# Kernel optimization log

Measured on AMD Instinct MI355X. Metric: run time of the kernel, lower is better.

The kernel has to match this reference:

```python
import jax, jax.numpy as jnp
import numpy as np

N = 100000   # nodes
E = 3200000  # edges
D = 16       # n_qubits / feature dim
H = 64       # classifier hidden
C = 10       # output_dims
L = 2        # len(q_depths)


def setup_inputs() -> dict:
    key = jax.random.key(0)
    ks = jax.random.split(key, 16)
    s = 1.0 / np.sqrt(D)
    return {
        "x": jax.random.normal(ks[0], (N, D), jnp.float32),
        "edge_index": jax.random.randint(ks[1], (2, E), 0, N, dtype=jnp.int32),
        "edge_attr": jax.random.uniform(ks[2], (E,), jnp.float32),
        "batch": jnp.zeros((N,), jnp.int32),
        # per-layer GCNConv params
        "lin_w": jax.random.uniform(ks[3], (L, D, D), jnp.float32, -s, s),
        "conv_b": jnp.zeros((L, D), jnp.float32),
        # per-layer nodeNN (stand-in for quantum_net): tanh(W x + b)
        "node_w": jax.random.uniform(ks[4], (L, D, D), jnp.float32, -s, s),
        "node_b": jnp.zeros((L, D), jnp.float32),
        # per-layer LayerNorm affine
        "ln_g": jnp.ones((L, D), jnp.float32),
        "ln_b": jnp.zeros((L, D), jnp.float32),
        # classifier
        "w1": jax.random.normal(ks[5], (H, D), jnp.float32) * np.sqrt(2.0 / (D + H)),
        "b1": jnp.zeros((H,), jnp.float32),
        "w2": jax.random.normal(ks[6], (C, H), jnp.float32) * np.sqrt(2.0 / (H + C)),
        "b2": jnp.zeros((C,), jnp.float32),
    }


def _layer_norm(h, g, b, eps=1e-5):
    mu = h.mean(-1, keepdims=True)
    var = ((h - mu) ** 2).mean(-1, keepdims=True)
    return (h - mu) * jax.lax.rsqrt(var + eps) * g + b


def reference(x, edge_index, edge_attr, batch, lin_w, conv_b, node_w, node_b,
              ln_g, ln_b, w1, b1, w2, b2):
    n = x.shape[0]
    # gcn_norm with add_self_loops=True (fill_value=1)
    loop = jnp.arange(n, dtype=edge_index.dtype)
    row = jnp.concatenate([edge_index[0], loop])  # source
    col = jnp.concatenate([edge_index[1], loop])  # target
    ew = jnp.concatenate([edge_attr, jnp.ones((n,), x.dtype)])
    deg = jax.ops.segment_sum(ew, col, num_segments=n)
    dinv = jnp.where(deg > 0, jax.lax.rsqrt(jnp.maximum(deg, 1e-30)), 0.0)
    norm = dinv[row] * ew * dinv[col]  # [E+N]

    h = x
    n_layers = lin_w.shape[0]
    for i in range(n_layers):
        out = h @ lin_w[i].T                      # lin (no bias)
        msg = norm[:, None] * out[row]            # gather + scale, [E+N, D]
        agg = jax.ops.segment_sum(msg, col, num_segments=n)  # scatter-add
        out = jnp.tanh(agg @ node_w[i].T + node_b[i])  # nodeNN update (quantum_net stand-in)
        out = out + conv_b[i]
        h = jnp.where(out > 0, out, 0.2 * out)    # LeakyReLU(0.2)
        h = _layer_norm(h, ln_g[i], ln_b[i])

    h = jax.nn.relu(h @ w1.T + b1)                # classifier (dropout = identity at eval)
    return h @ w2.T + b2
```

## Files before the change

### kernel.cpp

```cpp
#include <hip/hip_runtime.h>
#include <hip/hip_bf16.h>

namespace {

constexpr int N_NODES = 100000;
constexpr int N_EDGES = 3200000;
constexpr int D = 16;
constexpr int H = 64;
constexpr int C = 10;
constexpr int BLK = 256;
constexpr int BLKS = 512;
constexpr int NBN = (N_NODES + BLK - 1) / BLK;

constexpr int PA = 32;
constexpr int NP = (N_NODES + PA - 1) / PA;

constexpr int CBN = 256;
constexpr int NC = (N_NODES + CBN - 1) / CBN;
constexpr int NPTR = NC * CBN + 1;

constexpr int NBB = 1024;
constexpr int EC = N_EDGES / NBB;
constexpr int REC2_CAP = N_EDGES + 7 * N_NODES;

__device__ inline unsigned short f2bf(float f) {
  unsigned u = __float_as_uint(f);
  return (unsigned short)((u + 0x7FFFu + ((u >> 16) & 1u)) >> 16);
}
__device__ inline float bf2f(unsigned short b) {
  return __uint_as_float(((unsigned)b) << 16);
}

__global__ void k_bincount(const int* __restrict__ col, int* __restrict__ blk_hist) {
  __shared__ int lh[NC];
  for (int i = threadIdx.x; i < NC; i += BLKS) lh[i] = 0;
  __syncthreads();
  const int b = blockIdx.x;
  const int e0 = b * EC, e1 = e0 + EC;
  for (int e = e0 + threadIdx.x; e < e1; e += 4 * BLKS) {
    int cc[4]; bool ok[4];
#pragma unroll
    for (int j = 0; j < 4; ++j) {
      int ee = e + j * BLKS;
      ok[j] = ee < e1;
      cc[j] = ok[j] ? col[ee] : 0;
    }
#pragma unroll
    for (int j = 0; j < 4; ++j)
      if (ok[j]) atomicAdd(&lh[cc[j] >> 8], 1);
  }
  __syncthreads();
  for (int i = threadIdx.x; i < NC; i += BLKS)
    blk_hist[(size_t)b * NC + i] = lh[i];
}

__global__ void k_colscan(int* __restrict__ blk_hist, int* __restrict__ bin_cnt) {
  const int i = blockIdx.x;
  const int t = threadIdx.x;
  int v[4];
  int s = 0;
#pragma unroll
  for (int j = 0; j < 4; ++j) {
    v[j] = blk_hist[(size_t)(t * 4 + j) * NC + i];
    s += v[j];
  }
  const int lane = t & 63;
  int incl = s;
#pragma unroll
  for (int off = 1; off < 64; off <<= 1) {
    int y = __shfl_up(incl, off, 64);
    if (lane >= off) incl += y;
  }
  __shared__ int wsum[4];
  const int w = t >> 6;
  if (lane == 63) wsum[w] = incl;
  __syncthreads();
  int wbase = 0;
#pragma unroll
  for (int k = 0; k < 4; ++k) wbase += (k < w) ? wsum[k] : 0;
  int excl = wbase + incl - s;
#pragma unroll
  for (int j = 0; j < 4; ++j) {
    blk_hist[(size_t)(t * 4 + j) * NC + i] = excl;
    excl += v[j];
  }
  if (t == BLK - 1) bin_cnt[i] = excl;
}

__global__ void k_scan(const int* __restrict__ src, int* __restrict__ dst, int n,
                       int sentinel) {
  __shared__ int s0[2048], s1[2048];
  const int t = threadIdx.x;
  int v0 = (t < n) ? src[t] : 0;
  int v1 = (t + 1024 < n) ? src[t + 1024] : 0;
  s0[t] = v0; s0[t + 1024] = v1;
  __syncthreads();
  int* cur = s0; int* nxt = s1;
  for (int off = 1; off < 2048; off <<= 1) {
    nxt[t] = cur[t] + (t >= off ? cur[t - off] : 0);
    int i1 = t + 1024;
    nxt[i1] = cur[i1] + (i1 >= off ? cur[i1 - off] : 0);
    __syncthreads();
    int* tmp = cur; cur = nxt; nxt = tmp;
  }
  if (t < n) dst[t] = cur[t] - v0;
  if (t + 1024 < n) dst[t + 1024] = cur[t + 1024] - v1;
  if (t == 0 && sentinel >= 0) dst[n] = sentinel;
}

__global__ void k_binscatter(const int* __restrict__ row, const int* __restrict__ col,
                             const float* __restrict__ ew, const int* __restrict__ coarse_ptr,
                             const int* __restrict__ blk_hist, uint2* __restrict__ recs) {
  __shared__ int lcur[NC];
  const int b = blockIdx.x;
  for (int i = threadIdx.x; i < NC; i += BLKS)
    lcur[i] = coarse_ptr[i] + blk_hist[(size_t)b * NC + i];
  __syncthreads();
  const int e0 = b * EC, e1 = e0 + EC;
  for (int e = e0 + threadIdx.x; e < e1; e += 8 * BLKS) {
    int cc[8], rr[8]; float ww[8]; bool ok[8];
#pragma unroll
    for (int j = 0; j < 8; ++j) {
      int ee = e + j * BLKS;
      ok[j] = ee < e1;
      cc[j] = ok[j] ? col[ee] : 0;
      rr[j] = ok[j] ? row[ee] : 0;
      ww[j] = ok[j] ? ew[ee] : 0.f;
    }
#pragma unroll
    for (int j = 0; j < 8; ++j) {
      if (ok[j]) {
        int c = cc[j];
        int pos = atomicAdd(&lcur[c >> 8], 1);
        recs[pos] = make_uint2((unsigned)rr[j] | ((unsigned)(c & (CBN - 1)) << 17),
                               __float_as_uint(ww[j]));
      }
    }
  }
}

__global__ void k_cntnode(const uint2* __restrict__ recs, const int* __restrict__ coarse_ptr,
                          int* __restrict__ cnt_g, int* __restrict__ pad_cnt) {
  __shared__ int cnt[CBN];
  __shared__ int ws[4];
  const int b = blockIdx.x;
  const int tid = threadIdx.x;
  if (tid < CBN) cnt[tid] = 0;
  __syncthreads();
  const int beg = coarse_ptr[b], end = coarse_ptr[b + 1];
  for (int p = beg + tid; p < end; p += 4 * BLKS) {
    unsigned xx[4]; bool ok[4];
#pragma unroll
    for (int j = 0; j < 4; ++j) {
      int pp = p + j * BLKS;
      ok[j] = pp < end;
      xx[j] = ok[j] ? recs[pp].x : 0u;
    }
#pragma unroll
    for (int j = 0; j < 4; ++j)
      if (ok[j]) atomicAdd(&cnt[xx[j] >> 17], 1);
  }
  __syncthreads();
  if (tid < CBN) {
    int c = cnt[tid];
    cnt_g[b * CBN + tid] = c;
    int pv = (c + 7) & ~7;
#pragma unroll
    for (int m = 1; m < 64; m <<= 1) pv += __shfl_xor(pv, m, 64);
    if ((tid & 63) == 0) ws[tid >> 6] = pv;
  }
  __syncthreads();
  if (tid == 0) pad_cnt[b] = ws[0] + ws[1] + ws[2] + ws[3];
}

__global__ void k_sortscatter(const uint2* __restrict__ recs, const int* __restrict__ coarse_ptr,
                              const int* __restrict__ cnt_g, const int* __restrict__ pad_ptr,
                              int* __restrict__ node_ptr, uint2* __restrict__ recs2) {
  __shared__ int cur[CBN];
  __shared__ int fin[CBN];
  __shared__ int wsum[4];
  const int b = blockIdx.x;
  const int tid = threadIdx.x;
  int pc = 0, incl = 0;
  if (tid < CBN) {
    pc = (cnt_g[b * CBN + tid] + 7) & ~7;
    incl = pc;
    const int lane = tid & 63;
#pragma unroll
    for (int off = 1; off < 64; off <<= 1) {
      int y = __shfl_up(incl, off, 64);
      if (lane >= off) incl += y;
    }
    if (lane == 63) wsum[tid >> 6] = incl;
  }
  __syncthreads();
  if (tid < CBN) {
    const int w = tid >> 6;
    int wb = 0;
#pragma unroll
    for (int k = 0; k < 4; ++k) wb += (k < w) ? wsum[k] : 0;
    int excl = wb + incl - pc + pad_ptr[b];
    cur[tid] = excl;
    fin[tid] = excl + pc;
    node_ptr[b * CBN + tid] = excl;
    if (b == NC - 1 && tid == CBN - 1) node_ptr[NC * CBN] = excl + pc;
  }
  __syncthreads();
  const int beg = coarse_ptr[b], end = coarse_ptr[b + 1];
  for (int p = beg + tid; p < end; p += 4 * BLKS) {
    uint2 r[4]; bool ok[4];
#pragma unroll
    for (int j = 0; j < 4; ++j) {
      int pp = p + j * BLKS;
      ok[j] = pp < end;
      r[j] = ok[j] ? recs[pp] : make_uint2(0u, 0u);
    }
#pragma unroll
    for (int j = 0; j < 4; ++j) {
      if (ok[j]) {
        int pos = atomicAdd(&cur[r[j].x >> 17], 1);
        recs2[pos] = make_uint2(r[j].x & 0x1FFFF, r[j].y);
      }
    }
  }
  __syncthreads();
  if (tid < CBN) {
    for (int q = cur[tid]; q < fin[tid]; ++q) recs2[q] = make_uint2(0u, 0u);
  }
}

__global__ void k_dinv2(const int* __restrict__ node_ptr, const uint2* __restrict__ recs2,
                        float* __restrict__ dinv) {
  int v = blockIdx.x * BLK + threadIdx.x;
  if (v >= N_NODES) return;
  float s = 1.0f;
  int e = node_ptr[v + 1];
  for (int p = node_ptr[v]; p < e; ++p) s += __uint_as_float(recs2[p].y);
  dinv[v] = s > 0.f ? rsqrtf(fmaxf(s, 1e-30f)) : 0.f;
}

__global__ void k_lin(const float* __restrict__ hin, const float* __restrict__ W,
                      const float* __restrict__ dinv, unsigned short* __restrict__ outd) {
  __shared__ float sW[D * D];
  sW[threadIdx.x] = W[threadIdx.x];
  __syncthreads();
  int v = blockIdx.x * BLK + threadIdx.x;
  if (v >= N_NODES) return;
  float hv[D];
  const float4* hp = reinterpret_cast<const float4*>(hin + (size_t)v * D);
#pragma unroll
  for (int c = 0; c < 4; ++c) {
    float4 t = hp[c];
    hv[4 * c + 0] = t.x; hv[4 * c + 1] = t.y;
    hv[4 * c + 2] = t.z; hv[4 * c + 3] = t.w;
  }
  float dv = dinv[v];
  unsigned short ob[D];
#pragma unroll
  for (int j = 0; j < D; ++j) {
    float s = 0.f;
#pragma unroll
    for (int k = 0; k < D; ++k) s += hv[k] * sW[j * D + k];
    ob[j] = f2bf(s * dv);
  }
  uint4 w0, w1;
  w0.x = (unsigned)ob[0]  | ((unsigned)ob[1]  << 16);
  w0.y = (unsigned)ob[2]  | ((unsigned)ob[3]  << 16);
  w0.z = (unsigned)ob[4]  | ((unsigned)ob[5]  << 16);
  w0.w = (unsigned)ob[6]  | ((unsigned)ob[7]  << 16);
  w1.x = (unsigned)ob[8]  | ((unsigned)ob[9]  << 16);
  w1.y = (unsigned)ob[10] | ((unsigned)ob[11] << 16);
  w1.z = (unsigned)ob[12] | ((unsigned)ob[13] << 16);
  w1.w = (unsigned)ob[14] | ((unsigned)ob[15] << 16);
  uint4* op = reinterpret_cast<uint4*>(outd + (size_t)v * D);
  op[0] = w0;
  op[1] = w1;
}

template <int MODE>
__global__ void k_agg(const int* __restrict__ node_ptr, const uint2* __restrict__ recs2,
                      const float* __restrict__ dinv, const unsigned short* __restrict__ outd,
                      const float* __restrict__ Wn, const float* __restrict__ nb,
                      const float* __restrict__ cb, const float* __restrict__ lg,
                      const float* __restrict__ lb,
                      const float* __restrict__ Wlin_next,
                      unsigned short* __restrict__ outd_next,
                      const float* __restrict__ w1, const float* __restrict__ b1,
                      const float* __restrict__ w2, const float* __restrict__ b2,
                      float* __restrict__ outc) {
  __shared__ float sacc[PA * 17];
  __shared__ float sdinv[PA];
  __shared__ float sWT[D * D];
  __shared__ float snb[D], scb[D], slg[D], slb[D];
  __shared__ float sWT2[D * D];
  __shared__ float sw1[H * D];
  __shared__ float sb1[H];
  __shared__ float sw2[C * H];
  __shared__ float sb2[C];
  const int b = blockIdx.x;
  const int base = b * PA;
  const int tid = threadIdx.x;

  sWT[tid] = Wn[(tid & 15) * D + (tid >> 4)];
  if (tid < D) {
    snb[tid] = nb[tid]; scb[tid] = cb[tid];
    slg[tid] = lg[tid]; slb[tid] = lb[tid];
  }
  if constexpr (MODE == 1) {
    sWT2[tid] = Wlin_next[(tid & 15) * D + (tid >> 4)];
  }
  if constexpr (MODE == 2) {
    for (int i = tid; i < H * D; i += BLK) sw1[i] = w1[i];
    if (tid < H) sb1[tid] = b1[tid];
    for (int i = tid; i < C * H; i += BLK) sw2[i] = w2[i];
    if (tid < C) sb2[tid] = b2[tid];
  }
  if (tid < PA) {
    int v = base + tid;
    sdinv[tid] = (v < N_NODES) ? dinv[v] : 0.f;
  }
  __syncthreads();

  const int g = tid >> 4;
  const int l = tid & 15;
#pragma unroll
  for (int i = 0; i < PA / 16; ++i) {
    const int n = g + 16 * i;
    const int v = base + n;
    float acc = (v < N_NODES) ? bf2f(outd[(size_t)v * D + l]) : 0.f;
    int p = node_ptr[v];
    const int e = node_ptr[v + 1];
    uint4 a0, a1, a2, a3;
    if (p < e) {
      const uint4* rp = reinterpret_cast<const uint4*>(recs2 + p);
      a0 = rp[0]; a1 = rp[1]; a2 = rp[2]; a3 = rp[3];
    }
    for (; p < e; p += 8) {
      const int pn = (p + 8 < e) ? p + 8 : p;
      const uint4* rpn = reinterpret_cast<const uint4*>(recs2 + pn);
      uint4 b0 = rpn[0], b1_ = rpn[1], b2_ = rpn[2], b3 = rpn[3];
      float g0 = bf2f(outd[(size_t)a0.x * D + l]);
      float g1 = bf2f(outd[(size_t)a0.z * D + l]);
      float g2 = bf2f(outd[(size_t)a1.x * D + l]);
      float g3 = bf2f(outd[(size_t)a1.z * D + l]);
      float g4 = bf2f(outd[(size_t)a2.x * D + l]);
      float g5 = bf2f(outd[(size_t)a2.z * D + l]);
      float g6 = bf2f(outd[(size_t)a3.x * D + l]);
      float g7 = bf2f(outd[(size_t)a3.z * D + l]);
      acc = fmaf(__uint_as_float(a0.y), g0, acc);
      acc = fmaf(__uint_as_float(a0.w), g1, acc);
      acc = fmaf(__uint_as_float(a1.y), g2, acc);
      acc = fmaf(__uint_as_float(a1.w), g3, acc);
      acc = fmaf(__uint_as_float(a2.y), g4, acc);
      acc = fmaf(__uint_as_float(a2.w), g5, acc);
      acc = fmaf(__uint_as_float(a3.y), g6, acc);
      acc = fmaf(__uint_as_float(a3.w), g7, acc);
      a0 = b0; a1 = b1_; a2 = b2_; a3 = b3;
    }
    sacc[n * 17 + l] = acc;
  }
  __syncthreads();

#pragma unroll
  for (int nb0 = 0; nb0 < PA / 16; ++nb0) {
    int n = nb0 * 16 + g;
    int v = base + n;
    float s = 0.f;
#pragma unroll
    for (int k = 0; k < D; ++k) s += sacc[n * 17 + k] * sWT[k * D + l];
    s = snb[l] + sdinv[n] * s;
    float u = tanhf(s) + scb[l];
    u = u > 0.f ? u : 0.2f * u;
    float mu = u;
#pragma unroll
    for (int m = 1; m < 16; m <<= 1) mu += __shfl_xor(mu, m, 64);
    mu *= (1.0f / D);
    float dd = u - mu;
    float var = dd * dd;
#pragma unroll
    for (int m = 1; m < 16; m <<= 1) var += __shfl_xor(var, m, 64);
    var *= (1.0f / D);
    float inv = rsqrtf(var + 1e-5f);
    float hval = dd * inv * slg[l] + slb[l];

    sacc[n * 17 + l] = hval;

    if constexpr (MODE == 1) {
      float s2 = 0.f;
#pragma unroll
      for (int k = 0; k < D; ++k) s2 += sacc[n * 17 + k] * sWT2[k * D + l];
      if (v < N_NODES) outd_next[(size_t)v * D + l] = f2bf(s2 * sdinv[n]);
    } else {
      float po[C];
#pragma unroll
      for (int c = 0; c < C; ++c) po[c] = 0.f;
#pragma unroll
      for (int jj = 0; jj < 4; ++jj) {
        int j = l + 16 * jj;
        float t = sb1[j];
#pragma unroll
        for (int k = 0; k < D; ++k) t += sacc[n * 17 + k] * sw1[j * D + k];
        t = fmaxf(t, 0.f);
#pragma unroll
        for (int c = 0; c < C; ++c) po[c] += t * sw2[c * H + j];
      }
#pragma unroll
      for (int m = 1; m < 16; m <<= 1) {
#pragma unroll
        for (int c = 0; c < C; ++c) po[c] += __shfl_xor(po[c], m, 64);
      }
      float sel = 0.f;
#pragma unroll
      for (int c = 0; c < C; ++c) sel = (l == c) ? po[c] : sel;
      if (v < N_NODES && l < C) outc[(size_t)v * C + l] = sel + sb2[l];
    }
  }
}

inline char* align_up(char* p, size_t a) {
  return (char*)(((uintptr_t)p + a - 1) & ~(uintptr_t)(a - 1));
}

}

extern "C" void kernel_launch(void* const* d_in, const int* in_sizes, int n_in,
                              void* d_out, int out_size, void* d_ws, size_t ws_size,
                              hipStream_t stream) {
  const float* x         = (const float*)d_in[0];
  const int*   edge_idx  = (const int*)d_in[1];
  const float* edge_attr = (const float*)d_in[2];
  const float* lin_w  = (const float*)d_in[4];
  const float* conv_b = (const float*)d_in[5];
  const float* node_w = (const float*)d_in[6];
  const float* node_b = (const float*)d_in[7];
  const float* ln_g   = (const float*)d_in[8];
  const float* ln_b   = (const float*)d_in[9];
  const float* w1     = (const float*)d_in[10];
  const float* b1     = (const float*)d_in[11];
  const float* w2     = (const float*)d_in[12];
  const float* b2     = (const float*)d_in[13];
  float* out = (float*)d_out;

  const int* row = edge_idx;
  const int* col = edge_idx + N_EDGES;

  char* p = (char*)d_ws;
  int*   bin_cnt    = (int*)p;   p = align_up(p + sizeof(int) * NC, 256);
  int*   coarse_ptr = (int*)p;   p = align_up(p + sizeof(int) * (NC + 1), 256);
  int*   pad_cnt    = (int*)p;   p = align_up(p + sizeof(int) * NC, 256);
  int*   pad_ptr    = (int*)p;   p = align_up(p + sizeof(int) * (NC + 1), 256);
  int*   cnt_g      = (int*)p;   p = align_up(p + sizeof(int) * (size_t)(NC * CBN), 256);
  int*   node_ptr   = (int*)p;   p = align_up(p + sizeof(int) * (size_t)NPTR, 256);
  float* dinv       = (float*)p; p = align_up(p + sizeof(float) * N_NODES, 256);
  char*  recs_mem   = p;         p = align_up(p + sizeof(uint2) * (size_t)N_EDGES, 256);
  uint2* recs2      = (uint2*)p; p = align_up(p + sizeof(uint2) * (size_t)REC2_CAP, 256);

  uint2* recs = (uint2*)recs_mem;
  unsigned short* outbA = (unsigned short*)recs_mem;
  unsigned short* outbB = (unsigned short*)align_up(
      recs_mem + sizeof(unsigned short) * (size_t)N_NODES * D, 256);
  int* blk_hist = (int*)recs2;

  k_bincount<<<NBB, BLKS, 0, stream>>>(col, blk_hist);
  k_colscan<<<NC, BLK, 0, stream>>>(blk_hist, bin_cnt);
  k_scan<<<1, 1024, 0, stream>>>(bin_cnt, coarse_ptr, NC, N_EDGES);
  k_binscatter<<<NBB, BLKS, 0, stream>>>(row, col, edge_attr, coarse_ptr, blk_hist, recs);
  k_cntnode<<<NC, BLKS, 0, stream>>>(recs, coarse_ptr, cnt_g, pad_cnt);
  k_scan<<<1, 1024, 0, stream>>>(pad_cnt, pad_ptr, NC, -1);
  k_sortscatter<<<NC, BLKS, 0, stream>>>(recs, coarse_ptr, cnt_g, pad_ptr, node_ptr, recs2);
  k_dinv2<<<NBN, BLK, 0, stream>>>(node_ptr, recs2, dinv);

  k_lin<<<NBN, BLK, 0, stream>>>(x, lin_w, dinv, outbA);
  k_agg<1><<<NP, BLK, 0, stream>>>(node_ptr, recs2, dinv, outbA,
                                   node_w, node_b, conv_b, ln_g, ln_b,
                                   lin_w + D * D, outbB,
                                   nullptr, nullptr, nullptr, nullptr, nullptr);
  k_agg<2><<<NP, BLK, 0, stream>>>(node_ptr, recs2, dinv, outbB,
                                   node_w + D * D, node_b + D, conv_b + D,
                                   ln_g + D, ln_b + D,
                                   nullptr, nullptr,
                                   w1, b1, w2, b2, out);
}
```

Before: 192.7 us.

## Split classifier MLP out of final aggregation into separate per-node kernel

The final aggregation kernel no longer runs the classifier MLP. It writes the layer-normalized hidden state as bf16, and a new kernel then computes the 16→64→10 MLP with one thread per node. This cuts the aggregation kernel's shared memory and register use, which should raise occupancy for the latency-bound gather, and removes the cross-lane shuffle reduction of ten partial sums. The layer-1 next-layer matmul now gathers h through shuffles instead of a shared-memory round trip. The cost is an extra launch, a bf16 round trip of h through memory (a small precision loss before the classifier), and a serial 64×(16+10) FMA loop per thread.

```diff
diff --git a/kernel.cpp b/kernel.cpp
--- a/kernel.cpp
+++ b/kernel.cpp
@@ -284,19 +284,12 @@
                       const float* __restrict__ cb, const float* __restrict__ lg,
                       const float* __restrict__ lb,
                       const float* __restrict__ Wlin_next,
-                      unsigned short* __restrict__ outd_next,
-                      const float* __restrict__ w1, const float* __restrict__ b1,
-                      const float* __restrict__ w2, const float* __restrict__ b2,
-                      float* __restrict__ outc) {
+                      unsigned short* __restrict__ outd_next) {
   __shared__ float sacc[PA * 17];
   __shared__ float sdinv[PA];
   __shared__ float sWT[D * D];
   __shared__ float snb[D], scb[D], slg[D], slb[D];
-  __shared__ float sWT2[D * D];
-  __shared__ float sw1[H * D];
-  __shared__ float sb1[H];
-  __shared__ float sw2[C * H];
-  __shared__ float sb2[C];
+  __shared__ float sWT2[(MODE == 1) ? D * D : 1];
   const int b = blockIdx.x;
   const int base = b * PA;
   const int tid = threadIdx.x;
@@ -308,12 +301,6 @@
   }
   if constexpr (MODE == 1) {
     sWT2[tid] = Wlin_next[(tid & 15) * D + (tid >> 4)];
-  }
-  if constexpr (MODE == 2) {
-    for (int i = tid; i < H * D; i += BLK) sw1[i] = w1[i];
-    if (tid < H) sb1[tid] = b1[tid];
-    for (int i = tid; i < C * H; i += BLK) sw2[i] = w2[i];
-    if (tid < C) sb2[tid] = b2[tid];
   }
   if (tid < PA) {
     int v = base + tid;
@@ -383,38 +370,57 @@
     float inv = rsqrtf(var + 1e-5f);
     float hval = dd * inv * slg[l] + slb[l];
 
-    sacc[n * 17 + l] = hval;
-
-    if constexpr (MODE == 1) {
+    if constexpr (MODE == 0) {
+      if (v < N_NODES) outd_next[(size_t)v * D + l] = f2bf(hval);
+    } else {
+      float hreg[D];
+#pragma unroll
+      for (int k = 0; k < D; ++k) hreg[k] = __shfl(hval, k, 16);
       float s2 = 0.f;
 #pragma unroll
-      for (int k = 0; k < D; ++k) s2 += sacc[n * 17 + k] * sWT2[k * D + l];
+      for (int k = 0; k < D; ++k) s2 = fmaf(hreg[k], sWT2[k * D + l], s2);
       if (v < N_NODES) outd_next[(size_t)v * D + l] = f2bf(s2 * sdinv[n]);
-    } else {
-      float po[C];
-#pragma unroll
-      for (int c = 0; c < C; ++c) po[c] = 0.f;
-#pragma unroll
-      for (int jj = 0; jj < 4; ++jj) {
-        int j = l + 16 * jj;
-        float t = sb1[j];
-#pragma unroll
-        for (int k = 0; k < D; ++k) t += sacc[n * 17 + k] * sw1[j * D + k];
-        t = fmaxf(t, 0.f);
-#pragma unroll
-        for (int c = 0; c < C; ++c) po[c] += t * sw2[c * H + j];
-      }
-#pragma unroll
-      for (int m = 1; m < 16; m <<= 1) {
-#pragma unroll
-        for (int c = 0; c < C; ++c) po[c] += __shfl_xor(po[c], m, 64);
-      }
-      float sel = 0.f;
-#pragma unroll
-      for (int c = 0; c < C; ++c) sel = (l == c) ? po[c] : sel;
-      if (v < N_NODES && l < C) outc[(size_t)v * C + l] = sel + sb2[l];
-    }
-  }
+    }
+  }
+}
+
+__global__ void k_cls(const unsigned short* __restrict__ h, const float* __restrict__ w1,
+                      const float* __restrict__ b1, const float* __restrict__ w2,
+                      const float* __restrict__ b2, float* __restrict__ out) {
+  __shared__ float sw1[H * D];
+  __shared__ float sb1[H];
+  __shared__ float sw2[C * H];
+  __shared__ float sb2[C];
+  for (int i = threadIdx.x; i < H * D; i += BLK) sw1[i] = w1[i];
+  for (int i = threadIdx.x; i < H; i += BLK) sb1[i] = b1[i];
+  for (int i = threadIdx.x; i < C * H; i += BLK) sw2[i] = w2[i];
+  for (int i = threadIdx.x; i < C; i += BLK) sb2[i] = b2[i];
+  __syncthreads();
+  int v = blockIdx.x * BLK + threadIdx.x;
+  if (v >= N_NODES) return;
+  const uint4* hp = reinterpret_cast<const uint4*>(h + (size_t)v * D);
+  uint4 hb0 = hp[0], hb1 = hp[1];
+  float hv[D];
+  unsigned wrd[8] = {hb0.x, hb0.y, hb0.z, hb0.w, hb1.x, hb1.y, hb1.z, hb1.w};
+#pragma unroll
+  for (int c = 0; c < 8; ++c) {
+    hv[2 * c + 0] = bf2f((unsigned short)(wrd[c] & 0xFFFFu));
+    hv[2 * c + 1] = bf2f((unsigned short)(wrd[c] >> 16));
+  }
+  float oc[C];
+#pragma unroll
+  for (int c = 0; c < C; ++c) oc[c] = sb2[c];
+#pragma unroll
+  for (int j = 0; j < H; ++j) {
+    float s = sb1[j];
+#pragma unroll
+    for (int k = 0; k < D; ++k) s = fmaf(hv[k], sw1[j * D + k], s);
+    s = fmaxf(s, 0.f);
+#pragma unroll
+    for (int c = 0; c < C; ++c) oc[c] = fmaf(s, sw2[c * H + j], oc[c]);
+  }
+#pragma unroll
+  for (int c = 0; c < C; ++c) out[(size_t)v * C + c] = oc[c];
 }
 
 inline char* align_up(char* p, size_t a) {
@@ -473,11 +479,10 @@
   k_lin<<<NBN, BLK, 0, stream>>>(x, lin_w, dinv, outbA);
   k_agg<1><<<NP, BLK, 0, stream>>>(node_ptr, recs2, dinv, outbA,
                                    node_w, node_b, conv_b, ln_g, ln_b,
-                                   lin_w + D * D, outbB,
-                                   nullptr, nullptr, nullptr, nullptr, nullptr);
-  k_agg<2><<<NP, BLK, 0, stream>>>(node_ptr, recs2, dinv, outbB,
+                                   lin_w + D * D, outbB);
+  k_agg<0><<<NP, BLK, 0, stream>>>(node_ptr, recs2, dinv, outbB,
                                    node_w + D * D, node_b + D, conv_b + D,
                                    ln_g + D, ln_b + D,
-                                   nullptr, nullptr,
-                                   w1, b1, w2, b2, out);
-}
+                                   nullptr, outbA);
+  k_cls<<<NBN, BLK, 0, stream>>>(outbA, w1, b1, w2, b2, out);
+}
```

Result: faster. 188.7 us, median of 2 (-2.1%).
